# Optimization experiments

Hardware: AMD Instinct MI355X
Metric: run time of the kernel (lower is better)

## Reference

```python
import jax, jax.numpy as jnp
import numpy as np

LN_EPS = 1e-5


def setup_inputs() -> dict:
    key = jax.random.key(0)
    ks = jax.random.split(key, 4)
    B, S, H, R = 8, 4096, 1024, 64
    hidden_states = jax.random.normal(ks[0], (B, S, H), dtype=jnp.float32)
    w_down = jax.random.normal(ks[1], (H, R), dtype=jnp.float32) * (1.0 / np.sqrt(H))
    b_down = jnp.zeros((R,), dtype=jnp.float32)
    w_up = jax.random.normal(ks[2], (R, H), dtype=jnp.float32) * (1.0 / np.sqrt(R))
    b_up = jnp.zeros((H,), dtype=jnp.float32)
    ln_gamma = jnp.ones((H,), dtype=jnp.float32)
    ln_beta = jnp.zeros((H,), dtype=jnp.float32)
    return {
        "hidden_states": hidden_states,
        "ln_gamma": ln_gamma,
        "ln_beta": ln_beta,
        "w_down": w_down,
        "b_down": b_down,
        "w_up": w_up,
        "b_up": b_up,
    }


def _layernorm(x, gamma, beta):
    mu = jnp.mean(x, axis=-1, keepdims=True)
    var = jnp.mean(jnp.square(x - mu), axis=-1, keepdims=True)
    return (x - mu) * jax.lax.rsqrt(var + LN_EPS) * gamma + beta


def reference(hidden_states, ln_gamma, ln_beta, w_down, b_down, w_up, b_up):
    # pre-norm adapter: LN -> down-proj -> gelu -> up-proj -> +residual
    res = hidden_states
    h = _layernorm(hidden_states, ln_gamma, ln_beta)
    h = jnp.einsum("bsh,hr->bsr", h, w_down) + b_down
    h = jax.nn.gelu(h, approximate=False)  # torch GELU (exact erf form)
    h = jnp.einsum("bsr,rh->bsh", h, w_up) + b_up
    return h + res
```

## Files before the change

kernel.cpp:

```cpp
#include <hip/hip_runtime.h>
#include <hip/hip_bf16.h>
#include <math.h>

#define H 1024
#define R 64
#define BM 32
#define NTHREADS 256
#define TSTRIDE 72

typedef __attribute__((ext_vector_type(8))) short short8;
typedef __attribute__((ext_vector_type(4))) float floatx4;

__device__ __forceinline__ unsigned short f2bf(float f) {
    unsigned int u = __builtin_bit_cast(unsigned int, f);
    u += 0x7fffu + ((u >> 16) & 1u);
    return (unsigned short)(u >> 16);
}

__global__ void prep_weights(const float* __restrict__ w_down,
                             const float* __restrict__ w_up,
                             unsigned short* __restrict__ wsd,
                             unsigned short* __restrict__ wsu) {
    int tid = blockIdx.x * blockDim.x + threadIdx.x;
    int j    = tid & 7;
    int lane = (tid >> 3) & 63;
    int f    = tid >> 9;
    int b = lane >> 4, p = lane & 15;
    {
        int kk = f >> 2, n = f & 3;
        int row = kk * 32 + b * 8 + j;
        int col = n * 16 + p;
        wsd[tid] = f2bf(w_down[row * R + col]);
    }
    {
        int ks = f >> 6, n = f & 63;
        int row = ks * 32 + b * 8 + j;
        int col = n * 16 + p;
        wsu[tid] = f2bf(w_up[row * H + col]);
    }
}

__global__ __launch_bounds__(NTHREADS, 2)
void adapter_kernel(const float* __restrict__ x,
                    const float* __restrict__ gamma,
                    const float* __restrict__ beta,
                    const float* __restrict__ b_down,
                    const float* __restrict__ b_up,
                    const unsigned short* __restrict__ wsd,
                    const unsigned short* __restrict__ wsu,
                    float* __restrict__ out) {
    __shared__ __align__(16) unsigned short y_lds[BM * H];
    __shared__ __align__(16) unsigned short t_lds[BM * TSTRIDE];

    const int tid  = threadIdx.x;
    const int lane = tid & 63;
    const int wave = tid >> 6;
    const long rowbase = (long)blockIdx.x * BM;

    float gg[16], bb[16];
    {
        const floatx4* g4 = (const floatx4*)(gamma + lane * 16);
        const floatx4* b4 = (const floatx4*)(beta  + lane * 16);
        #pragma unroll
        for (int q = 0; q < 4; ++q) {
            floatx4 gv = g4[q], bv = b4[q];
            #pragma unroll
            for (int e = 0; e < 4; ++e) { gg[q*4+e] = gv[e]; bb[q*4+e] = bv[e]; }
        }
    }
    #pragma unroll 2
    for (int i = 0; i < 8; ++i) {
        int r = wave * 8 + i;
        const floatx4* xr = (const floatx4*)(x + (rowbase + r) * H + lane * 16);
        float v[16];
        #pragma unroll
        for (int q = 0; q < 4; ++q) {
            floatx4 xv = xr[q];
            #pragma unroll
            for (int e = 0; e < 4; ++e) v[q*4+e] = xv[e];
        }
        float s1 = 0.f, s2 = 0.f;
        #pragma unroll
        for (int q = 0; q < 16; ++q) { s1 += v[q]; s2 += v[q] * v[q]; }
        #pragma unroll
        for (int off = 32; off >= 1; off >>= 1) {
            s1 += __shfl_xor(s1, off);
            s2 += __shfl_xor(s2, off);
        }
        float mu  = s1 * (1.0f / (float)H);
        float var = s2 * (1.0f / (float)H) - mu * mu;
        float rs  = rsqrtf(var + 1e-5f);
        int c = r & 7;
        short8 lo, hi;
        #pragma unroll
        for (int q = 0; q < 8; ++q) lo[q] = (short)f2bf((v[q]     - mu) * rs * gg[q]     + bb[q]);
        #pragma unroll
        for (int q = 0; q < 8; ++q) hi[q] = (short)f2bf((v[q + 8] - mu) * rs * gg[q + 8] + bb[q + 8]);
        int s0 = (2 * lane)     ^ c;
        int s1g = (2 * lane + 1) ^ c;
        *(short8*)&y_lds[r * H + s0  * 8] = lo;
        *(short8*)&y_lds[r * H + s1g * 8] = hi;
    }
    __syncthreads();

    const int g = wave >> 1;
    const int c = wave & 1;
    const int p = lane & 15;
    const int b = lane >> 4;

    floatx4 acc0 = {0.f, 0.f, 0.f, 0.f};
    floatx4 acc1 = {0.f, 0.f, 0.f, 0.f};
    const int arow = 16 * g + p;
    const int asw  = arow & 7;
    const short8* wsd8 = (const short8*)wsd;
    #pragma unroll 4
    for (int kk = 0; kk < 32; ++kk) {
        int gidx = 4 * kk + b;
        short8 a  = *(const short8*)&y_lds[arow * H + ((gidx ^ asw) * 8)];
        short8 b0 = wsd8[(kk * 4 + 2 * c)     * 64 + lane];
        short8 b1 = wsd8[(kk * 4 + 2 * c + 1) * 64 + lane];
        acc0 = __builtin_amdgcn_mfma_f32_16x16x32_bf16(a, b0, acc0, 0, 0, 0);
        acc1 = __builtin_amdgcn_mfma_f32_16x16x32_bf16(a, b1, acc1, 0, 0, 0);
    }
    {
        float bd0 = b_down[32 * c + p];
        float bd1 = b_down[32 * c + 16 + p];
        #pragma unroll
        for (int reg = 0; reg < 4; ++reg) {
            int trow = 16 * g + b * 4 + reg;
            float u0 = acc0[reg] + bd0;
            float u1 = acc1[reg] + bd1;
            u0 = 0.5f * u0 * (1.0f + erff(u0 * 0.70710678f));
            u1 = 0.5f * u1 * (1.0f + erff(u1 * 0.70710678f));
            t_lds[trow * TSTRIDE + 32 * c + p]      = f2bf(u0);
            t_lds[trow * TSTRIDE + 32 * c + 16 + p] = f2bf(u1);
        }
    }
    __syncthreads();

    const int arow3 = 16 * g + p;
    short8 a0 = *(const short8*)&t_lds[arow3 * TSTRIDE + b * 8];
    short8 a1 = *(const short8*)&t_lds[arow3 * TSTRIDE + 32 + b * 8];
    const short8* wsu8 = (const short8*)wsu;
    const long rb = rowbase + 16 * g;

    #pragma unroll 2
    for (int nn = 0; nn < 32; ++nn) {
        int n = 32 * c + nn;
        short8 bu0 = wsu8[(n)      * 64 + lane];
        short8 bu1 = wsu8[(64 + n) * 64 + lane];
        floatx4 acc = {0.f, 0.f, 0.f, 0.f};
        acc = __builtin_amdgcn_mfma_f32_16x16x32_bf16(a0, bu0, acc, 0, 0, 0);
        acc = __builtin_amdgcn_mfma_f32_16x16x32_bf16(a1, bu1, acc, 0, 0, 0);
        int col = n * 16 + p;
        float bup = b_up[col];
        #pragma unroll
        for (int reg = 0; reg < 4; ++reg) {
            long rr = rb + b * 4 + reg;
            out[rr * H + col] = acc[reg] + bup + x[rr * H + col];
        }
    }
}

extern "C" void kernel_launch(void* const* d_in, const int* in_sizes, int n_in,
                              void* d_out, int out_size, void* d_ws, size_t ws_size,
                              hipStream_t stream) {
    const float* x      = (const float*)d_in[0];
    const float* gamma  = (const float*)d_in[1];
    const float* beta   = (const float*)d_in[2];
    const float* w_down = (const float*)d_in[3];
    const float* b_down = (const float*)d_in[4];
    const float* w_up   = (const float*)d_in[5];
    const float* b_up   = (const float*)d_in[6];
    float* out = (float*)d_out;

    unsigned short* wsd = (unsigned short*)d_ws;
    unsigned short* wsu = wsd + 65536;

    int M = in_sizes[0] / H;
    prep_weights<<<256, 256, 0, stream>>>(w_down, w_up, wsd, wsu);
    adapter_kernel<<<M / BM, NTHREADS, 0, stream>>>(x, gamma, beta, b_down, b_up,
                                                    wsd, wsu, out);
}
```

Before: 271.6 us.

## Halve rows per block to 16 and remap waves across output columns

Block tile shrinks from 32 to 16 rows and the launch bound rises to 4 blocks per CU, so LDS use per block halves and more blocks can be resident. In the down-projection each of the four waves now owns one 16-column slice of R, and in the up-projection each wave owns a quarter of the H columns. The goal is higher occupancy and more blocks to hide memory latency in this bandwidth-bound kernel. In exchange, every block reloads the full weight set for half as many rows, which doubles weight traffic from L2 per row.

```diff
diff --git a/kernel.cpp b/kernel.cpp
--- a/kernel.cpp
+++ b/kernel.cpp
@@ -4,7 +4,7 @@
 
 #define H 1024
 #define R 64
-#define BM 32
+#define BM 16
 #define NTHREADS 256
 #define TSTRIDE 72
 
@@ -40,7 +40,7 @@
     }
 }
 
-__global__ __launch_bounds__(NTHREADS, 2)
+__global__ __launch_bounds__(NTHREADS, 4)
 void adapter_kernel(const float* __restrict__ x,
                     const float* __restrict__ gamma,
                     const float* __restrict__ beta,
@@ -69,8 +69,8 @@
         }
     }
     #pragma unroll 2
-    for (int i = 0; i < 8; ++i) {
-        int r = wave * 8 + i;
+    for (int i = 0; i < 4; ++i) {
+        int r = wave * 4 + i;
         const floatx4* xr = (const floatx4*)(x + (rowbase + r) * H + lane * 16);
         float v[16];
         #pragma unroll
@@ -96,68 +96,56 @@
         for (int q = 0; q < 8; ++q) lo[q] = (short)f2bf((v[q]     - mu) * rs * gg[q]     + bb[q]);
         #pragma unroll
         for (int q = 0; q < 8; ++q) hi[q] = (short)f2bf((v[q + 8] - mu) * rs * gg[q + 8] + bb[q + 8]);
-        int s0 = (2 * lane)     ^ c;
+        int s0  = (2 * lane)     ^ c;
         int s1g = (2 * lane + 1) ^ c;
         *(short8*)&y_lds[r * H + s0  * 8] = lo;
         *(short8*)&y_lds[r * H + s1g * 8] = hi;
     }
     __syncthreads();
 
-    const int g = wave >> 1;
-    const int c = wave & 1;
     const int p = lane & 15;
     const int b = lane >> 4;
 
-    floatx4 acc0 = {0.f, 0.f, 0.f, 0.f};
-    floatx4 acc1 = {0.f, 0.f, 0.f, 0.f};
-    const int arow = 16 * g + p;
-    const int asw  = arow & 7;
+    floatx4 acc = {0.f, 0.f, 0.f, 0.f};
+    const int asw = p & 7;
     const short8* wsd8 = (const short8*)wsd;
     #pragma unroll 4
     for (int kk = 0; kk < 32; ++kk) {
         int gidx = 4 * kk + b;
-        short8 a  = *(const short8*)&y_lds[arow * H + ((gidx ^ asw) * 8)];
-        short8 b0 = wsd8[(kk * 4 + 2 * c)     * 64 + lane];
-        short8 b1 = wsd8[(kk * 4 + 2 * c + 1) * 64 + lane];
-        acc0 = __builtin_amdgcn_mfma_f32_16x16x32_bf16(a, b0, acc0, 0, 0, 0);
-        acc1 = __builtin_amdgcn_mfma_f32_16x16x32_bf16(a, b1, acc1, 0, 0, 0);
+        short8 a  = *(const short8*)&y_lds[p * H + ((gidx ^ asw) * 8)];
+        short8 b0 = wsd8[(kk * 4 + wave) * 64 + lane];
+        acc = __builtin_amdgcn_mfma_f32_16x16x32_bf16(a, b0, acc, 0, 0, 0);
     }
     {
-        float bd0 = b_down[32 * c + p];
-        float bd1 = b_down[32 * c + 16 + p];
+        float bd = b_down[16 * wave + p];
         #pragma unroll
         for (int reg = 0; reg < 4; ++reg) {
-            int trow = 16 * g + b * 4 + reg;
-            float u0 = acc0[reg] + bd0;
-            float u1 = acc1[reg] + bd1;
-            u0 = 0.5f * u0 * (1.0f + erff(u0 * 0.70710678f));
-            u1 = 0.5f * u1 * (1.0f + erff(u1 * 0.70710678f));
-            t_lds[trow * TSTRIDE + 32 * c + p]      = f2bf(u0);
-            t_lds[trow * TSTRIDE + 32 * c + 16 + p] = f2bf(u1);
+            int trow = b * 4 + reg;
+            float u = acc[reg] + bd;
+            u = 0.5f * u * (1.0f + erff(u * 0.70710678f));
+            t_lds[trow * TSTRIDE + 16 * wave + p] = f2bf(u);
         }
     }
     __syncthreads();
 
-    const int arow3 = 16 * g + p;
-    short8 a0 = *(const short8*)&t_lds[arow3 * TSTRIDE + b * 8];
-    short8 a1 = *(const short8*)&t_lds[arow3 * TSTRIDE + 32 + b * 8];
+    short8 a0 = *(const short8*)&t_lds[p * TSTRIDE + b * 8];
+    short8 a1 = *(const short8*)&t_lds[p * TSTRIDE + 32 + b * 8];
     const short8* wsu8 = (const short8*)wsu;
-    const long rb = rowbase + 16 * g;
 
     #pragma unroll 2
-    for (int nn = 0; nn < 32; ++nn) {
-        int n = 32 * c + nn;
+    for (int nn = 0; nn < 16; ++nn) {
+        int n = 16 * wave + nn;
         short8 bu0 = wsu8[(n)      * 64 + lane];
         short8 bu1 = wsu8[(64 + n) * 64 + lane];
-        floatx4 acc = {0.f, 0.f, 0.f, 0.f};
-        acc = __builtin_amdgcn_mfma_f32_16x16x32_bf16(a0, bu0, acc, 0, 0, 0);
-        acc = __builtin_amdgcn_mfma_f32_16x16x32_bf16(a1, bu1, acc, 0, 0, 0);
+        floatx4 av = {0.f, 0.f, 0.f, 0.f};
+        av = __builtin_amdgcn_mfma_f32_16x16x32_bf16(a0, bu0, av, 0, 0, 0);
+        av = __builtin_amdgcn_mfma_f32_16x16x32_bf16(a1, bu1, av, 0, 0, 0);
         int col = n * 16 + p;
         float bup = b_up[col];
         #pragma unroll
         for (int reg = 0; reg < 4; ++reg) {
-            long rr = rb + b * 4 + reg;
-            out[rr * H + col] = acc[reg] + bup + x[rr * H + col];
+            long rr = rowbase + b * 4 + reg;
+            out[rr * H + col] = av[reg] + bup + x[rr * H + col];
         }
     }
 }
```

Measured after the change: 268.7 us. No clear change (-1.1%).
